# Kernel tuning notes

Measured on AMD Instinct MI355X. Metric: run time of the kernel, lower is better.

## Reference

```python
import jax, jax.numpy as jnp
import numpy as np

N = 100000
E = 3200000
F_IN = 256
HID = 128


def _dconv_k1(x_cat, w, b):
    # torch_geometric_temporal DConv with K=1:
    # H = X @ W[0,0] + X @ W[1,0] + b   (no graph propagation for K=1)
    return x_cat @ (w[0, 0] + w[1, 0]) + b


def _dcrnn_cell(x, h, wz, bz, wr, br, wh, bh):
    xh = jnp.concatenate([x, h], axis=1)
    z = jax.nn.sigmoid(_dconv_k1(xh, wz, bz))
    r = jax.nn.sigmoid(_dconv_k1(xh, wr, br))
    xrh = jnp.concatenate([x, r * h], axis=1)
    h_tilde = jnp.tanh(_dconv_k1(xrh, wh, bh))
    return z * h + (1.0 - z) * h_tilde


def setup_inputs() -> dict:
    key = jax.random.key(0)
    ks = jax.random.split(key, 16)

    def gw(k, shape):
        fan_in = shape[-2]
        return jax.random.normal(k, shape, dtype=jnp.float32) / np.sqrt(fan_in)

    inp = {
        "x": jax.random.normal(ks[0], (N, F_IN), dtype=jnp.float32),
        "edge_index": jax.random.randint(ks[1], (2, E), 0, N, dtype=jnp.int64 if jax.config.jax_enable_x64 else jnp.int32),
        "edge_weight": jax.random.uniform(ks[2], (E,), dtype=jnp.float32),
        "w_z1": gw(ks[3], (2, 1, F_IN + HID, HID)), "b_z1": jnp.zeros((HID,), jnp.float32),
        "w_r1": gw(ks[4], (2, 1, F_IN + HID, HID)), "b_r1": jnp.zeros((HID,), jnp.float32),
        "w_h1": gw(ks[5], (2, 1, F_IN + HID, HID)), "b_h1": jnp.zeros((HID,), jnp.float32),
        "w_z2": gw(ks[6], (2, 1, HID + HID // 2, HID // 2)), "b_z2": jnp.zeros((HID // 2,), jnp.float32),
        "w_r2": gw(ks[7], (2, 1, HID + HID // 2, HID // 2)), "b_r2": jnp.zeros((HID // 2,), jnp.float32),
        "w_h2": gw(ks[8], (2, 1, HID + HID // 2, HID // 2)), "b_h2": jnp.zeros((HID // 2,), jnp.float32),
        "w_lin1": gw(ks[9], (HID // 2, 16)), "b_lin1": jnp.zeros((16,), jnp.float32),
        "w_lin2": gw(ks[10], (16, 1)), "b_lin2": jnp.zeros((1,), jnp.float32),
    }
    return inp


def reference(x, edge_index, edge_weight,
              w_z1, b_z1, w_r1, b_r1, w_h1, b_h1,
              w_z2, b_z2, w_r2, b_r2, w_h2, b_h2,
              w_lin1, b_lin1, w_lin2, b_lin2):
    # edge_index / edge_weight are unused in the K=1 DConv math (faithful to tgt source).
    h0 = jnp.zeros((x.shape[0], w_z1.shape[-1]), x.dtype)
    h = _dcrnn_cell(x, h0, w_z1, b_z1, w_r1, b_r1, w_h1, b_h1)
    h = jax.nn.relu(h)
    h0b = jnp.zeros((x.shape[0], w_z2.shape[-1]), x.dtype)
    h = _dcrnn_cell(h, h0b, w_z2, b_z2, w_r2, b_r2, w_h2, b_h2)
    h = jax.nn.relu(h)
    # Dropout(0.2) is identity at inference
    h = jax.nn.relu(h @ w_lin1 + b_lin1)
    return h @ w_lin2 + b_lin2
```

## Files before the change

kernel.cpp:

```cpp
#include <hip/hip_runtime.h>

typedef _Float16 f16;
typedef _Float16 f16x4 __attribute__((ext_vector_type(4)));
typedef _Float16 f16x8 __attribute__((ext_vector_type(8)));
typedef float    f32x4 __attribute__((ext_vector_type(4)));

#define N_ROWS 100000
#define RT 1563
#define LSX 264
#define LSH1 136
#define LSH2 72

#define W1F_OFF 0
#define W1F_BYTES (256 * 256 * 2)
#define W2F_OFF W1F_BYTES

#define ARENA 33792
#define H1S 0
#define H2S 17408

__global__ void prep_w(const float* __restrict__ wz1, const float* __restrict__ wh1,
                       const float* __restrict__ wz2, const float* __restrict__ wh2,
                       f16* __restrict__ W1F, f16* __restrict__ W2F) {
    const int b = blockIdx.x, tid = threadIdx.x;
    if (b < 32) {
        int idx = b * 256 + tid;
        int l = idx & 63, itm = idx >> 6;
        int it = itm & 7, M = itm >> 3;
        int ln = l & 15, q = l >> 4;
        int col = M * 16 + ln;
        int k0 = it * 32 + q * 8;
        const float* w = (col < 128) ? wz1 : wh1;
        int cc = col & 127;
        f16x8 v;
#pragma unroll
        for (int j = 0; j < 8; ++j) {
            int k = k0 + j;
            v[j] = (f16)(w[k * 128 + cc] + w[384 * 128 + k * 128 + cc]);
        }
        *(f16x8*)&W1F[idx * 8] = v;
    } else {
        int idx = (b - 32) * 256 + tid;
        if (idx >= 2048) return;
        int l = idx & 63, tkc = idx >> 6;
        int kc = tkc & 3, t = tkc >> 2;
        int ln = l & 15, q = l >> 4;
        int col = (t < 4) ? (16 * t + ln) : (64 + 16 * (t - 4) + ln);
        int k0 = kc * 32 + q * 8;
        const float* w = (col < 64) ? wz2 : wh2;
        int cc = col & 63;
        f16x8 v;
#pragma unroll
        for (int j = 0; j < 8; ++j) {
            int k = k0 + j;
            v[j] = (f16)(w[k * 64 + cc] + w[192 * 64 + k * 64 + cc]);
        }
        *(f16x8*)&W2F[idx * 8] = v;
    }
}

__device__ __forceinline__ float gate(float zp, float hp) {
    float e2h = __expf(2.0f * fminf(hp, 15.0f));
    float ez  = __expf(zp);
    float r   = __builtin_amdgcn_rcpf((e2h + 1.0f) * (1.0f + ez));
    return fmaxf((e2h - 1.0f) * r, 0.0f);
}

__global__ __launch_bounds__(256, 4) void fused(
    const float* __restrict__ x,
    const f16* __restrict__ W1F, const f16* __restrict__ W2F,
    const float* __restrict__ bz1, const float* __restrict__ bh1,
    const float* __restrict__ bz2, const float* __restrict__ bh2,
    const float* __restrict__ wl1, const float* __restrict__ bl1,
    const float* __restrict__ wl2, const float* __restrict__ bl2,
    float* __restrict__ out)
{
    __shared__ __align__(16) char arena[ARENA];
    const int tid = threadIdx.x, lane = tid & 63, wave = tid >> 6;
    const int ln = lane & 15, quad = lane >> 4;
    const int r0 = blockIdx.x * 64;

    const int xr = tid >> 2, xcg = tid & 3;
    int gxr = r0 + xr; if (gxr >= N_ROWS) gxr = N_ROWS - 1;
    const float* xp = x + (size_t)gxr * 256 + (xcg << 3);

    f16* Xs = (f16*)arena;

#pragma unroll
    for (int half = 0; half < 2; ++half) {
        float4 xa[4], xb[4];
#pragma unroll
        for (int kc = 0; kc < 4; ++kc) {
            xa[kc] = *(const float4*)(xp + (half * 4 + kc) * 32);
            xb[kc] = *(const float4*)(xp + (half * 4 + kc) * 32 + 4);
        }
#pragma unroll
        for (int kc = 0; kc < 4; ++kc) {
            *(f16x8*)&Xs[xr * LSX + (half * 4 + kc) * 32 + (xcg << 3)] =
                (f16x8){(f16)xa[kc].x,(f16)xa[kc].y,(f16)xa[kc].z,(f16)xa[kc].w,
                        (f16)xb[kc].x,(f16)xb[kc].y,(f16)xb[kc].z,(f16)xb[kc].w};
        }
    }

    const int Mz = 2 * wave;
    const f16* wb[4];
#pragma unroll
    for (int mi = 0; mi < 4; ++mi) {
        const int M = (mi < 2) ? (Mz + mi) : (8 + Mz + mi - 2);
        wb[mi] = W1F + ((size_t)(M * 8) * 64 + lane) * 8;
    }

    __syncthreads();

    f32x4 acc[4][4];
#pragma unroll
    for (int a = 0; a < 4; ++a)
#pragma unroll
        for (int b = 0; b < 4; ++b) acc[a][b] = (f32x4){0.f, 0.f, 0.f, 0.f};

#pragma unroll
    for (int it = 0; it < 8; ++it) {
        f16x8 af[4], bf[4];
#pragma unroll
        for (int mi = 0; mi < 4; ++mi)
            af[mi] = *(const f16x8*)(wb[mi] + it * 512);
#pragma unroll
        for (int nt = 0; nt < 4; ++nt)
            bf[nt] = *(const f16x8*)&Xs[(16 * nt + ln) * LSX + it * 32 + quad * 8];
#pragma unroll
        for (int mi = 0; mi < 4; ++mi)
#pragma unroll
            for (int nt = 0; nt < 4; ++nt)
                acc[mi][nt] = __builtin_amdgcn_mfma_f32_16x16x32_f16(af[mi], bf[nt], acc[mi][nt], 0, 0, 0);
    }
    __syncthreads();

    f16x8 w2f[2][4];
#pragma unroll
    for (int kc = 0; kc < 4; ++kc) {
        w2f[0][kc] = *(const f16x8*)(W2F + ((size_t)((wave    ) * 4 + kc) * 64 + lane) * 8);
        w2f[1][kc] = *(const f16x8*)(W2F + ((size_t)((wave + 4) * 4 + kc) * 64 + lane) * 8);
    }

    f16* h1s = (f16*)(arena + H1S);
#pragma unroll
    for (int mi = 0; mi < 2; ++mi) {
        const int jg0 = 32 * wave + 16 * mi + (quad << 2);
        const float4 zb = *(const float4*)(bz1 + jg0);
        const float4 hb = *(const float4*)(bh1 + jg0);
#pragma unroll
        for (int nt = 0; nt < 4; ++nt) {
            const int row = 16 * nt + ln;
            f16x4 pk;
#pragma unroll
            for (int i = 0; i < 4; ++i)
                pk[i] = (f16)gate(acc[mi][nt][i] + (&zb.x)[i],
                                  acc[mi + 2][nt][i] + (&hb.x)[i]);
            *(f16x4*)&h1s[row * LSH1 + jg0] = pk;
        }
    }
    __syncthreads();

    f32x4 acc2[2][4];
#pragma unroll
    for (int a = 0; a < 2; ++a)
#pragma unroll
        for (int b = 0; b < 4; ++b) acc2[a][b] = (f32x4){0.f, 0.f, 0.f, 0.f};
#pragma unroll
    for (int kc = 0; kc < 4; ++kc) {
        f16x8 bf[4];
#pragma unroll
        for (int nt = 0; nt < 4; ++nt)
            bf[nt] = *(const f16x8*)&h1s[(16 * nt + ln) * LSH1 + kc * 32 + quad * 8];
#pragma unroll
        for (int m = 0; m < 2; ++m)
#pragma unroll
            for (int nt = 0; nt < 4; ++nt)
                acc2[m][nt] = __builtin_amdgcn_mfma_f32_16x16x32_f16(w2f[m][kc], bf[nt], acc2[m][nt], 0, 0, 0);
    }

    f16* h2s = (f16*)(arena + H2S);
    {
        const int jg0 = 16 * wave + (quad << 2);
        const float4 zb = *(const float4*)(bz2 + jg0);
        const float4 hb = *(const float4*)(bh2 + jg0);
#pragma unroll
        for (int nt = 0; nt < 4; ++nt) {
            const int row = 16 * nt + ln;
            f16x4 pk;
#pragma unroll
            for (int i = 0; i < 4; ++i)
                pk[i] = (f16)gate(acc2[0][nt][i] + (&zb.x)[i],
                                  acc2[1][nt][i] + (&hb.x)[i]);
            *(f16x4*)&h2s[row * LSH2 + jg0] = pk;
        }
    }
    __syncthreads();

    const float blv = bl1[ln], wlv = wl2[ln], bl2v = bl2[0];
    f16x8 bfr[2];
#pragma unroll
    for (int kc = 0; kc < 2; ++kc)
#pragma unroll
        for (int j = 0; j < 8; ++j)
            bfr[kc][j] = (f16)wl1[(32 * kc + 8 * quad + j) * 16 + ln];

    f32x4 acc3 = (f32x4){0.f, 0.f, 0.f, 0.f};
#pragma unroll
    for (int kc = 0; kc < 2; ++kc) {
        f16x8 af = *(const f16x8*)&h2s[(16 * wave + ln) * LSH2 + kc * 32 + quad * 8];
        acc3 = __builtin_amdgcn_mfma_f32_16x16x32_f16(af, bfr[kc], acc3, 0, 0, 0);
    }
#pragma unroll
    for (int i = 0; i < 4; ++i) {
        float v = fmaxf(acc3[i] + blv, 0.0f) * wlv;
        v += __shfl_xor(v, 1);
        v += __shfl_xor(v, 2);
        v += __shfl_xor(v, 4);
        v += __shfl_xor(v, 8);
        if (ln == 0) {
            const int row = r0 + 16 * wave + (quad << 2) + i;
            if (row < N_ROWS) out[row] = v + bl2v;
        }
    }
}

extern "C" void kernel_launch(void* const* d_in, const int* in_sizes, int n_in,
                              void* d_out, int out_size, void* d_ws, size_t ws_size,
                              hipStream_t stream) {
    const float* x   = (const float*)d_in[0];
    const float* wz1 = (const float*)d_in[3];
    const float* bz1 = (const float*)d_in[4];
    const float* wh1 = (const float*)d_in[7];
    const float* bh1 = (const float*)d_in[8];
    const float* wz2 = (const float*)d_in[9];
    const float* bz2 = (const float*)d_in[10];
    const float* wh2 = (const float*)d_in[13];
    const float* bh2 = (const float*)d_in[14];
    const float* wl1 = (const float*)d_in[15];
    const float* bl1 = (const float*)d_in[16];
    const float* wl2 = (const float*)d_in[17];
    const float* bl2 = (const float*)d_in[18];

    char* ws = (char*)d_ws;
    f16* W1F = (f16*)(ws + W1F_OFF);
    f16* W2F = (f16*)(ws + W2F_OFF);
    float* out = (float*)d_out;

    prep_w<<<40, 256, 0, stream>>>(wz1, wh1, wz2, wh2, W1F, W2F);
    fused<<<RT, 256, 0, stream>>>(x, W1F, W2F, bz1, bh1, bz2, bh2,
                                  wl1, bl1, wl2, bl2, out);
}
```

Before: 229.3 us.

## Double rows per block to 128 with 512 threads and per-wave column tiles

Each block now processes 128 rows with 8 waves. In the first GEMM each wave owns one z and one h column tile across all 8 row tiles, so one weight fragment pair is reused over more MFMAs, replacing the old 4x4 tile per wave. The second-layer work is split between waves by column group and row half. The x staging loads become nontemporal. The risks are a 64-entry accumulator array under launch_bounds(512,4), which may force spills, and doubled LDS per block, which limits resident blocks per CU.

New measurement: 221.4 us. 3.5% less time.

```diff
diff --git a/kernel.cpp b/kernel.cpp
--- a/kernel.cpp
+++ b/kernel.cpp
@@ -6,7 +6,8 @@
 typedef float    f32x4 __attribute__((ext_vector_type(4)));
 
 #define N_ROWS 100000
-#define RT 1563
+#define RT 782
+#define TPB 512
 #define LSX 264
 #define LSH1 136
 #define LSH2 72
@@ -15,9 +16,9 @@
 #define W1F_BYTES (256 * 256 * 2)
 #define W2F_OFF W1F_BYTES
 
-#define ARENA 33792
+#define ARENA 67584
 #define H1S 0
-#define H2S 17408
+#define H2S 34816
 
 __global__ void prep_w(const float* __restrict__ wz1, const float* __restrict__ wh1,
                        const float* __restrict__ wz2, const float* __restrict__ wh2,
@@ -66,7 +67,7 @@
     return fmaxf((e2h - 1.0f) * r, 0.0f);
 }
 
-__global__ __launch_bounds__(256, 4) void fused(
+__global__ __launch_bounds__(TPB, 4) void fused(
     const float* __restrict__ x,
     const f16* __restrict__ W1F, const f16* __restrict__ W2F,
     const float* __restrict__ bz1, const float* __restrict__ bh1,
@@ -78,84 +79,71 @@
     __shared__ __align__(16) char arena[ARENA];
     const int tid = threadIdx.x, lane = tid & 63, wave = tid >> 6;
     const int ln = lane & 15, quad = lane >> 4;
-    const int r0 = blockIdx.x * 64;
+    const int r0 = blockIdx.x * 128;
 
     const int xr = tid >> 2, xcg = tid & 3;
     int gxr = r0 + xr; if (gxr >= N_ROWS) gxr = N_ROWS - 1;
     const float* xp = x + (size_t)gxr * 256 + (xcg << 3);
 
     f16* Xs = (f16*)arena;
-
-#pragma unroll
-    for (int half = 0; half < 2; ++half) {
-        float4 xa[4], xb[4];
-#pragma unroll
-        for (int kc = 0; kc < 4; ++kc) {
-            xa[kc] = *(const float4*)(xp + (half * 4 + kc) * 32);
-            xb[kc] = *(const float4*)(xp + (half * 4 + kc) * 32 + 4);
-        }
-#pragma unroll
-        for (int kc = 0; kc < 4; ++kc) {
-            *(f16x8*)&Xs[xr * LSX + (half * 4 + kc) * 32 + (xcg << 3)] =
-                (f16x8){(f16)xa[kc].x,(f16)xa[kc].y,(f16)xa[kc].z,(f16)xa[kc].w,
-                        (f16)xb[kc].x,(f16)xb[kc].y,(f16)xb[kc].z,(f16)xb[kc].w};
-        }
-    }
-
-    const int Mz = 2 * wave;
-    const f16* wb[4];
-#pragma unroll
-    for (int mi = 0; mi < 4; ++mi) {
-        const int M = (mi < 2) ? (Mz + mi) : (8 + Mz + mi - 2);
-        wb[mi] = W1F + ((size_t)(M * 8) * 64 + lane) * 8;
-    }
-
-    __syncthreads();
-
-    f32x4 acc[4][4];
-#pragma unroll
-    for (int a = 0; a < 4; ++a)
-#pragma unroll
-        for (int b = 0; b < 4; ++b) acc[a][b] = (f32x4){0.f, 0.f, 0.f, 0.f};
+#pragma unroll 2
+    for (int kc = 0; kc < 8; ++kc) {
+        f32x4 a = __builtin_nontemporal_load((const f32x4*)(xp + kc * 32));
+        f32x4 b = __builtin_nontemporal_load((const f32x4*)(xp + kc * 32 + 4));
+        *(f16x8*)&Xs[xr * LSX + kc * 32 + (xcg << 3)] =
+            (f16x8){(f16)a[0],(f16)a[1],(f16)a[2],(f16)a[3],
+                    (f16)b[0],(f16)b[1],(f16)b[2],(f16)b[3]};
+    }
+
+    const f16* wbz = W1F + ((size_t)(wave * 8) * 64 + lane) * 8;
+    const f16* wbh = W1F + ((size_t)((wave + 8) * 8) * 64 + lane) * 8;
+
+    __syncthreads();
+
+    f32x4 acc[2][8];
+#pragma unroll
+    for (int a = 0; a < 2; ++a)
+#pragma unroll
+        for (int b = 0; b < 8; ++b) acc[a][b] = (f32x4){0.f, 0.f, 0.f, 0.f};
 
 #pragma unroll
     for (int it = 0; it < 8; ++it) {
-        f16x8 af[4], bf[4];
-#pragma unroll
-        for (int mi = 0; mi < 4; ++mi)
-            af[mi] = *(const f16x8*)(wb[mi] + it * 512);
-#pragma unroll
-        for (int nt = 0; nt < 4; ++nt)
+        f16x8 afz = *(const f16x8*)(wbz + it * 512);
+        f16x8 afh = *(const f16x8*)(wbh + it * 512);
+        f16x8 bf[8];
+#pragma unroll
+        for (int nt = 0; nt < 8; ++nt)
             bf[nt] = *(const f16x8*)&Xs[(16 * nt + ln) * LSX + it * 32 + quad * 8];
 #pragma unroll
-        for (int mi = 0; mi < 4; ++mi)
-#pragma unroll
-            for (int nt = 0; nt < 4; ++nt)
-                acc[mi][nt] = __builtin_amdgcn_mfma_f32_16x16x32_f16(af[mi], bf[nt], acc[mi][nt], 0, 0, 0);
-    }
-    __syncthreads();
-
+        for (int nt = 0; nt < 8; ++nt)
+            acc[0][nt] = __builtin_amdgcn_mfma_f32_16x16x32_f16(afz, bf[nt], acc[0][nt], 0, 0, 0);
+#pragma unroll
+        for (int nt = 0; nt < 8; ++nt)
+            acc[1][nt] = __builtin_amdgcn_mfma_f32_16x16x32_f16(afh, bf[nt], acc[1][nt], 0, 0, 0);
+    }
+    __syncthreads();
+
+    const int c = wave & 3, rh = wave >> 2;
     f16x8 w2f[2][4];
 #pragma unroll
     for (int kc = 0; kc < 4; ++kc) {
-        w2f[0][kc] = *(const f16x8*)(W2F + ((size_t)((wave    ) * 4 + kc) * 64 + lane) * 8);
-        w2f[1][kc] = *(const f16x8*)(W2F + ((size_t)((wave + 4) * 4 + kc) * 64 + lane) * 8);
+        w2f[0][kc] = *(const f16x8*)(W2F + ((size_t)((c    ) * 4 + kc) * 64 + lane) * 8);
+        w2f[1][kc] = *(const f16x8*)(W2F + ((size_t)((c + 4) * 4 + kc) * 64 + lane) * 8);
     }
 
     f16* h1s = (f16*)(arena + H1S);
-#pragma unroll
-    for (int mi = 0; mi < 2; ++mi) {
-        const int jg0 = 32 * wave + 16 * mi + (quad << 2);
+    {
+        const int jg0 = 16 * wave + (quad << 2);
         const float4 zb = *(const float4*)(bz1 + jg0);
         const float4 hb = *(const float4*)(bh1 + jg0);
 #pragma unroll
-        for (int nt = 0; nt < 4; ++nt) {
+        for (int nt = 0; nt < 8; ++nt) {
             const int row = 16 * nt + ln;
             f16x4 pk;
 #pragma unroll
             for (int i = 0; i < 4; ++i)
-                pk[i] = (f16)gate(acc[mi][nt][i] + (&zb.x)[i],
-                                  acc[mi + 2][nt][i] + (&hb.x)[i]);
+                pk[i] = (f16)gate(acc[0][nt][i] + (&zb.x)[i],
+                                  acc[1][nt][i] + (&hb.x)[i]);
             *(f16x4*)&h1s[row * LSH1 + jg0] = pk;
         }
     }
@@ -171,7 +159,7 @@
         f16x8 bf[4];
 #pragma unroll
         for (int nt = 0; nt < 4; ++nt)
-            bf[nt] = *(const f16x8*)&h1s[(16 * nt + ln) * LSH1 + kc * 32 + quad * 8];
+            bf[nt] = *(const f16x8*)&h1s[(16 * (4 * rh + nt) + ln) * LSH1 + kc * 32 + quad * 8];
 #pragma unroll
         for (int m = 0; m < 2; ++m)
 #pragma unroll
@@ -181,12 +169,12 @@
 
     f16* h2s = (f16*)(arena + H2S);
     {
-        const int jg0 = 16 * wave + (quad << 2);
+        const int jg0 = 16 * c + (quad << 2);
         const float4 zb = *(const float4*)(bz2 + jg0);
         const float4 hb = *(const float4*)(bh2 + jg0);
 #pragma unroll
         for (int nt = 0; nt < 4; ++nt) {
-            const int row = 16 * nt + ln;
+            const int row = 16 * (4 * rh + nt) + ln;
             f16x4 pk;
 #pragma unroll
             for (int i = 0; i < 4; ++i)
@@ -248,6 +236,6 @@
     float* out = (float*)d_out;
 
     prep_w<<<40, 256, 0, stream>>>(wz1, wh1, wz2, wh2, W1F, W2F);
-    fused<<<RT, 256, 0, stream>>>(x, W1F, W2F, bz1, bh1, bz2, bh2,
+    fused<<<RT, TPB, 0, stream>>>(x, W1F, W2F, bz1, bh1, bz2, bh2,
                                   wl1, bl1, wl2, bl2, out);
 }
```
